# Kernel tuning notes

Measured on AMD Instinct MI355X. Metric: run time of the kernel, lower is better.

Reference implementation:

```python
import jax, jax.numpy as jnp
import numpy as np

H_IN = 1024
H_OUT = 1024
P = 512
DT_MIN = 0.004
DT_MAX = 0.1
STEP_RESCALE = 1.0
MIN_NEG = 1e-3
EPS_LAM = 1e-6
EPS_DIV = 1e-9
CLIP_MAX = 20.0


def _hippo_lambda_raw(p):
    # Mirrors TorchS5.__init__ HiPPO-LegS-style symmetric init.
    idx = np.arange(p, dtype=np.float64)
    Pv = np.sqrt(1.0 + 2.0 * idx)
    A = np.tril(Pv[:, None] * Pv[None, :]) - np.diag(idx)
    A = -A
    Pr = np.sqrt(idx + 0.5)
    S = A + Pr[:, None] * Pr[None, :]
    S_sym = 0.5 * (S + S.T)
    eig = np.linalg.eigvalsh(S_sym).astype(np.float32)
    lambda_init = -np.clip(np.abs(eig), 1e-3, None)
    raw = -np.log(np.expm1(np.clip(-lambda_init, 1e-6, None)))
    return jnp.asarray(raw, dtype=jnp.float32)


def setup_inputs() -> dict:
    key = jax.random.key(0)
    ku, kt, kb, kc = jax.random.split(key, 4)
    Bsz, L = 16, 1024
    u = jax.random.normal(ku, (Bsz, L, H_IN), dtype=jnp.float32)
    timesteps = jax.random.uniform(kt, (Bsz, L), dtype=jnp.float32)
    Lambda_raw = _hippo_lambda_raw(P)
    log_step_init = 0.5 * (np.log(DT_MIN) + np.log(DT_MAX))
    log_step = jnp.full((P,), log_step_init, dtype=jnp.float32)
    # kaiming_uniform_(a=sqrt(5)) -> U(-1/sqrt(fan_in), 1/sqrt(fan_in))
    Bmat = jax.random.uniform(kb, (P, H_IN), dtype=jnp.float32,
                              minval=-1.0, maxval=1.0) / np.sqrt(H_IN)
    Cmat = jax.random.uniform(kc, (H_OUT, P), dtype=jnp.float32,
                              minval=-1.0, maxval=1.0) / np.sqrt(P)
    Dvec = jnp.zeros((H_IN,), dtype=jnp.float32)  # H_in == H_out path
    return {"u": u, "timesteps": timesteps, "Lambda_raw": Lambda_raw,
            "log_step": log_step, "B": Bmat, "C": Cmat, "D": Dvec}


def reference(u, timesteps, Lambda_raw, log_step, B, C, D):
    # u: [B,L,H_in], timesteps: [B,L]
    Bu = jnp.einsum('ph,blh->blp', B, u)                      # [B,L,P]
    step_vec = STEP_RESCALE * jnp.exp(log_step)               # [P]
    Lam = -(jax.nn.softplus(Lambda_raw) + MIN_NEG)            # [P]
    Delta = jnp.maximum(step_vec[None, None, :] * timesteps[..., None], 0.0)
    A_bar = jnp.exp(jnp.minimum(Lam[None, None, :] * Delta, CLIP_MAX))
    # zoh gamma: (exp(Lam*Delta)-1)/Lam, fallback Delta near Lam=0
    gamma = jnp.where(jnp.abs(Lam)[None, None, :] > EPS_LAM,
                      (A_bar - 1.0) / Lam[None, None, :], Delta)
    b_seq = gamma * Bu
    A_cum = jnp.cumprod(A_bar, axis=1)                        # [B,L,P]
    z = b_seq / (A_cum + EPS_DIV)
    s = jnp.cumsum(z, axis=1)
    x_seq = A_cum * s
    ys = jnp.einsum('hp,blp->blh', C, x_seq) + D * u          # [B,L,H_out]
    return ys
```

## Files before the change

### kernel.cpp

```cpp
#include <hip/hip_runtime.h>
#include <cstdint>
#include <cstddef>

#define H_IN   1024
#define H_OUTD 1024
#define PDIM   512
#define BSZ    16
#define LSEQ   1024
#define BLM    (BSZ * LSEQ)
#define CCH    32
#define CLEN   32

typedef __bf16 bf16_t;
typedef __bf16 bf16x8 __attribute__((ext_vector_type(8)));
typedef float  floatx4 __attribute__((ext_vector_type(4)));

__device__ __forceinline__ unsigned short f2bf(float f) {
    unsigned u = __float_as_uint(f);
    u = u + 0x7fffu + ((u >> 16) & 1u);
    return (unsigned short)(u >> 16);
}
__device__ __forceinline__ float bf2f(unsigned short s) {
    return __uint_as_float((unsigned)s << 16);
}

__device__ __forceinline__ void gl_lds16(const void* g, void* l) {
    __builtin_amdgcn_global_load_lds(
        (const __attribute__((address_space(1))) void*)g,
        (__attribute__((address_space(3))) void*)l, 16, 0, 0);
}

#define NU4 (BLM * H_IN / 4)
#define NB4 (PDIM * H_IN / 4)
#define NC4 (H_OUTD * PDIM / 4)
__global__ void setup_kernel(const float* __restrict__ Lraw,
                             const float* __restrict__ lstep,
                             float* __restrict__ stepv,
                             float* __restrict__ lamv,
                             const float4* __restrict__ Usrc,
                             ushort4* __restrict__ Udst,
                             const float4* __restrict__ Bsrc,
                             ushort4* __restrict__ Bdst,
                             const float4* __restrict__ Csrc,
                             ushort4* __restrict__ Cdst) {
    const int gid = blockIdx.x * 256 + threadIdx.x;
    if (gid < PDIM) {
        stepv[gid] = expf(lstep[gid]);
        float x = Lraw[gid];
        float sp = fmaxf(x, 0.0f) + log1pf(expf(-fabsf(x)));
        lamv[gid] = -(sp + 1e-3f);
    }
    if (gid < NU4) {
        float4 v = Usrc[gid];
        ushort4 o;
        o.x = f2bf(v.x); o.y = f2bf(v.y); o.z = f2bf(v.z); o.w = f2bf(v.w);
        Udst[gid] = o;
    } else {
        const int g2 = gid - NU4;
        if (g2 < NB4) {
            float4 v = Bsrc[g2];
            ushort4 o;
            o.x = f2bf(v.x); o.y = f2bf(v.y); o.z = f2bf(v.z); o.w = f2bf(v.w);
            Bdst[g2] = o;
        } else if (g2 < NB4 + NC4) {
            const int g3 = g2 - NB4;
            float4 v = Csrc[g3];
            ushort4 o;
            o.x = f2bf(v.x); o.y = f2bf(v.y); o.z = f2bf(v.z); o.w = f2bf(v.w);
            Cdst[g3] = o;
        }
    }
}

template<int EPI, int OUTBF, int GXL>
__global__ __launch_bounds__(256, 4)
void gemm_nt(const bf16_t* __restrict__ A, const bf16_t* __restrict__ Bm,
             float* __restrict__ Cf, unsigned short* __restrict__ Cb,
             int M, int N, int K,
             const float* __restrict__ Dv, const unsigned short* __restrict__ U) {
    __shared__ bf16_t As[2 * 128 * 32];
    __shared__ bf16_t Bs[2 * 128 * 32];

    const int i     = blockIdx.x;
    const int n_blk = (i >> 3) & ((1 << GXL) - 1);
    const int m_blk = ((i >> (3 + GXL)) << 3) | (i & 7);
    const int m0    = m_blk << 7;
    const int n0    = n_blk << 7;

    const int tid  = threadIdx.x;
    const int lane = tid & 63;
    const int w    = tid >> 6;
    const int wm   = (w & 1) << 6;
    const int wn   = (w >> 1) << 6;
    const int r16  = lane & 15;
    const int q    = lane >> 4;
    const int fsw  = (q ^ (r16 & 3)) << 3;

    const int srow = lane >> 2;
    const int seg  = (lane & 3) ^ (srow & 3);
    const int c0   = w * 32;
    const int c1   = c0 + 16;

    const bf16_t* gA0 = A  + (size_t)(m0 + c0 + srow) * K + seg * 8;
    const bf16_t* gA1 = A  + (size_t)(m0 + c1 + srow) * K + seg * 8;
    const bf16_t* gB0 = Bm + (size_t)(n0 + c0 + srow) * K + seg * 8;
    const bf16_t* gB1 = Bm + (size_t)(n0 + c1 + srow) * K + seg * 8;
    bf16_t* lA0 = &As[c0 * 32];
    bf16_t* lA1 = &As[c1 * 32];
    bf16_t* lB0 = &Bs[c0 * 32];
    bf16_t* lB1 = &Bs[c1 * 32];

    floatx4 acc[4][4] = {};

    gl_lds16(gA0, lA0);
    gl_lds16(gA1, lA1);
    gl_lds16(gB0, lB0);
    gl_lds16(gB1, lB1);
    __syncthreads();

    int cur = 0;
    for (int k0 = 0; k0 < K; k0 += 32) {
        const int nxt = cur ^ 1;
        if (k0 + 32 < K) {
            gl_lds16(gA0 + k0 + 32, lA0 + nxt * 4096);
            gl_lds16(gA1 + k0 + 32, lA1 + nxt * 4096);
            gl_lds16(gB0 + k0 + 32, lB0 + nxt * 4096);
            gl_lds16(gB1 + k0 + 32, lB1 + nxt * 4096);
        }

        const bf16_t* rA = As + cur * 4096;
        const bf16_t* rB = Bs + cur * 4096;
        bf16x8 af[4], bfr[4];
#pragma unroll
        for (int ii = 0; ii < 4; ++ii) {
            af[ii]  = *(const bf16x8*)&rA[(wm + ii * 16 + r16) * 32 + fsw];
            bfr[ii] = *(const bf16x8*)&rB[(wn + ii * 16 + r16) * 32 + fsw];
        }
#pragma unroll
        for (int mi = 0; mi < 4; ++mi)
#pragma unroll
            for (int ni = 0; ni < 4; ++ni)
                acc[mi][ni] = __builtin_amdgcn_mfma_f32_16x16x32_bf16(
                    af[mi], bfr[ni], acc[mi][ni], 0, 0, 0);

        __syncthreads();
        cur = nxt;
    }

    float dn[4];
    if (EPI == 1) {
#pragma unroll
        for (int ni = 0; ni < 4; ++ni) dn[ni] = Dv[n0 + wn + ni * 16 + r16];
    }
#pragma unroll
    for (int mi = 0; mi < 4; ++mi) {
#pragma unroll
        for (int e = 0; e < 4; ++e) {
            const int m = m0 + wm + mi * 16 + q * 4 + e;
#pragma unroll
            for (int ni = 0; ni < 4; ++ni) {
                const int n = n0 + wn + ni * 16 + r16;
                const size_t idx = (size_t)m * N + n;
                float v = acc[mi][ni][e];
                if (EPI == 1) v += dn[ni] * bf2f(U[idx]);
                if (OUTBF == 1) Cb[idx] = f2bf(v);
                else            Cf[idx] = v;
            }
        }
    }
}

__global__ __launch_bounds__(512)
void scan_part1(const unsigned short* __restrict__ Bu, const float* __restrict__ ts,
                const float* __restrict__ stepv, const float* __restrict__ lamv,
                float* __restrict__ Pagg, float* __restrict__ Sagg) {
    const int c = blockIdx.x;
    const int b = blockIdx.y;
    const int p = threadIdx.x;

    const float lam  = lamv[p];
    const float stp  = stepv[p];
    const float rlam = 1.0f / lam;
    const bool  lam_big = fabsf(lam) > 1e-6f;

    const unsigned short* bu = Bu + ((size_t)b * LSEQ + c * CLEN) * PDIM + p;
    const float* tb = ts + b * LSEQ + c * CLEN;

    float P = 1.0f, S = 0.0f;
#pragma unroll 8
    for (int i = 0; i < CLEN; ++i) {
        float t     = tb[i];
        float delta = fmaxf(stp * t, 0.0f);
        float e     = fminf(lam * delta, 20.0f);
        float abar  = __expf(e);
        float gamma = lam_big ? (abar - 1.0f) * rlam : delta;
        S = fmaf(abar, S, gamma * bf2f(bu[(size_t)i * PDIM]));
        P *= abar;
    }
    const size_t o = ((size_t)b * CCH + c) * PDIM + p;
    Pagg[o] = P;
    Sagg[o] = S;
}

__global__ __launch_bounds__(512)
void scan_part23(const unsigned short* __restrict__ Bu, const float* __restrict__ ts,
                 const float* __restrict__ stepv, const float* __restrict__ lamv,
                 const float* __restrict__ Pagg, const float* __restrict__ Sagg,
                 unsigned short* __restrict__ Xbf) {
    const int c = blockIdx.x;
    const int b = blockIdx.y;
    const int p = threadIdx.x;

    const float lam  = lamv[p];
    const float stp  = stepv[p];
    const float rlam = 1.0f / lam;
    const bool  lam_big = fabsf(lam) > 1e-6f;

    const float* Pb = Pagg + (size_t)b * CCH * PDIM + p;
    const float* Sb = Sagg + (size_t)b * CCH * PDIM + p;
    float x = 0.0f;
    int cc = 0;
    for (; cc + 4 <= c; cc += 4) {
        float p0 = Pb[(size_t)(cc + 0) * PDIM], s0 = Sb[(size_t)(cc + 0) * PDIM];
        float p1 = Pb[(size_t)(cc + 1) * PDIM], s1 = Sb[(size_t)(cc + 1) * PDIM];
        float p2 = Pb[(size_t)(cc + 2) * PDIM], s2 = Sb[(size_t)(cc + 2) * PDIM];
        float p3 = Pb[(size_t)(cc + 3) * PDIM], s3 = Sb[(size_t)(cc + 3) * PDIM];
        float p01 = p0 * p1, s01 = fmaf(s0, p1, s1);
        float p23 = p2 * p3, s23 = fmaf(s2, p3, s3);
        float pq  = p01 * p23, sq = fmaf(s01, p23, s23);
        x = fmaf(pq, x, sq);
    }
    for (; cc < c; ++cc) {
        x = fmaf(Pb[(size_t)cc * PDIM], x, Sb[(size_t)cc * PDIM]);
    }

    const unsigned short* bu = Bu + ((size_t)b * LSEQ + c * CLEN) * PDIM + p;
    const float* tb = ts + b * LSEQ + c * CLEN;
    unsigned short* xo = Xbf + ((size_t)b * LSEQ + c * CLEN) * PDIM + p;

#pragma unroll 8
    for (int i = 0; i < CLEN; ++i) {
        float t     = tb[i];
        float delta = fmaxf(stp * t, 0.0f);
        float e     = fminf(lam * delta, 20.0f);
        float abar  = __expf(e);
        float gamma = lam_big ? (abar - 1.0f) * rlam : delta;
        x = fmaf(abar, x, gamma * bf2f(bu[(size_t)i * PDIM]));
        xo[(size_t)i * PDIM] = f2bf(x);
    }
}

extern "C" void kernel_launch(void* const* d_in, const int* in_sizes, int n_in,
                              void* d_out, int out_size, void* d_ws, size_t ws_size,
                              hipStream_t stream) {
    (void)in_sizes; (void)n_in; (void)out_size; (void)ws_size;
    const float* u  = (const float*)d_in[0];
    const float* ts = (const float*)d_in[1];
    const float* Lr = (const float*)d_in[2];
    const float* ls = (const float*)d_in[3];
    const float* Bm = (const float*)d_in[4];
    const float* Cm = (const float*)d_in[5];
    const float* Dv = (const float*)d_in[6];
    float* out = (float*)d_out;

    char* ws = (char*)d_ws;
    bf16_t*         u_bf = (bf16_t*)(ws);
    bf16_t*         B_bf = (bf16_t*)(ws + (32u << 20));
    bf16_t*         C_bf = (bf16_t*)(ws + (33u << 20));
    unsigned short* Bu   = (unsigned short*)(ws + (34u << 20));
    unsigned short* X_bf = (unsigned short*)(ws + (50u << 20));
    float*          Pagg = (float*)(ws + (66u << 20));
    float*          Sagg = (float*)(ws + (67u << 20));
    float*          stepv= (float*)(ws + (69u << 20));
    float*          lamv = stepv + PDIM;

    setup_kernel<<<(NU4 + NB4 + NC4) / 256, 256, 0, stream>>>(
        Lr, ls, stepv, lamv,
        (const float4*)u,  (ushort4*)u_bf,
        (const float4*)Bm, (ushort4*)B_bf,
        (const float4*)Cm, (ushort4*)C_bf);

    gemm_nt<0, 1, 2><<<512, 256, 0, stream>>>(
        u_bf, B_bf, nullptr, Bu, BLM, PDIM, H_IN, nullptr, nullptr);

    scan_part1<<<dim3(CCH, BSZ), 512, 0, stream>>>(Bu, ts, stepv, lamv, Pagg, Sagg);
    scan_part23<<<dim3(CCH, BSZ), 512, 0, stream>>>(Bu, ts, stepv, lamv,
                                                    Pagg, Sagg, X_bf);

    gemm_nt<1, 0, 3><<<1024, 256, 0, stream>>>(
        (const bf16_t*)X_bf, C_bf, out, nullptr, BLM, H_OUTD, PDIM, Dv,
        (const unsigned short*)u_bf);
}
```

Baseline: 192.8 us.

## Triple-buffer GEMM LDS tiles with prefetch depth two and skip zero-D epilogue loads

```diff
diff --git a/kernel.cpp b/kernel.cpp
--- a/kernel.cpp
+++ b/kernel.cpp
@@ -73,13 +73,13 @@
 }
 
 template<int EPI, int OUTBF, int GXL>
-__global__ __launch_bounds__(256, 4)
+__global__ __launch_bounds__(256, 3)
 void gemm_nt(const bf16_t* __restrict__ A, const bf16_t* __restrict__ Bm,
              float* __restrict__ Cf, unsigned short* __restrict__ Cb,
              int M, int N, int K,
              const float* __restrict__ Dv, const unsigned short* __restrict__ U) {
-    __shared__ bf16_t As[2 * 128 * 32];
-    __shared__ bf16_t Bs[2 * 128 * 32];
+    __shared__ bf16_t As[3 * 4096];
+    __shared__ bf16_t Bs[3 * 4096];
 
     const int i     = blockIdx.x;
     const int n_blk = (i >> 3) & ((1 << GXL) - 1);
@@ -112,24 +112,38 @@
 
     floatx4 acc[4][4] = {};
 
+    const int nk = K >> 5;
+
     gl_lds16(gA0, lA0);
     gl_lds16(gA1, lA1);
     gl_lds16(gB0, lB0);
     gl_lds16(gB1, lB1);
-    __syncthreads();
-
-    int cur = 0;
-    for (int k0 = 0; k0 < K; k0 += 32) {
-        const int nxt = cur ^ 1;
-        if (k0 + 32 < K) {
-            gl_lds16(gA0 + k0 + 32, lA0 + nxt * 4096);
-            gl_lds16(gA1 + k0 + 32, lA1 + nxt * 4096);
-            gl_lds16(gB0 + k0 + 32, lB0 + nxt * 4096);
-            gl_lds16(gB1 + k0 + 32, lB1 + nxt * 4096);
+    {
+        const int off = 32;
+        gl_lds16(gA0 + off, lA0 + 4096);
+        gl_lds16(gA1 + off, lA1 + 4096);
+        gl_lds16(gB0 + off, lB0 + 4096);
+        gl_lds16(gB1 + off, lB1 + 4096);
+    }
+
+    int rd = 0;
+    int wr = 2;
+    for (int kk = 0; kk < nk; ++kk) {
+        if (kk + 1 < nk) asm volatile("s_waitcnt vmcnt(4)" ::: "memory");
+        else             asm volatile("s_waitcnt vmcnt(0)" ::: "memory");
+        __builtin_amdgcn_s_barrier();
+
+        if (kk + 2 < nk) {
+            const int off = (kk + 2) << 5;
+            gl_lds16(gA0 + off, lA0 + wr * 4096);
+            gl_lds16(gA1 + off, lA1 + wr * 4096);
+            gl_lds16(gB0 + off, lB0 + wr * 4096);
+            gl_lds16(gB1 + off, lB1 + wr * 4096);
+            wr = (wr + 1 == 3) ? 0 : wr + 1;
         }
 
-        const bf16_t* rA = As + cur * 4096;
-        const bf16_t* rB = Bs + cur * 4096;
+        const bf16_t* rA = As + rd * 4096;
+        const bf16_t* rB = Bs + rd * 4096;
         bf16x8 af[4], bfr[4];
 #pragma unroll
         for (int ii = 0; ii < 4; ++ii) {
@@ -143,8 +157,7 @@
                 acc[mi][ni] = __builtin_amdgcn_mfma_f32_16x16x32_bf16(
                     af[mi], bfr[ni], acc[mi][ni], 0, 0, 0);
 
-        __syncthreads();
-        cur = nxt;
+        rd = (rd + 1 == 3) ? 0 : rd + 1;
     }
 
     float dn[4];
@@ -162,7 +175,9 @@
                 const int n = n0 + wn + ni * 16 + r16;
                 const size_t idx = (size_t)m * N + n;
                 float v = acc[mi][ni][e];
-                if (EPI == 1) v += dn[ni] * bf2f(U[idx]);
+                if (EPI == 1) {
+                    if (dn[ni] != 0.0f) v += dn[ni] * bf2f(U[idx]);
+                }
                 if (OUTBF == 1) Cb[idx] = f2bf(v);
                 else            Cf[idx] = v;
             }
```

After: 194.6 us. Within noise of the previous version (+0.9%).

## Fuse fp32-to-bf16 conversion of u into the first GEMM's A-tile load

Applied to the files above, without the earlier changes.

```diff
diff --git a/kernel.cpp b/kernel.cpp
--- a/kernel.cpp
+++ b/kernel.cpp
@@ -23,6 +23,9 @@
 __device__ __forceinline__ float bf2f(unsigned short s) {
     return __uint_as_float((unsigned)s << 16);
 }
+__device__ __forceinline__ unsigned pk2(float lo, float hi) {
+    return (unsigned)f2bf(lo) | ((unsigned)f2bf(hi) << 16);
+}
 
 __device__ __forceinline__ void gl_lds16(const void* g, void* l) {
     __builtin_amdgcn_global_load_lds(
@@ -30,15 +33,12 @@
         (__attribute__((address_space(3))) void*)l, 16, 0, 0);
 }
 
-#define NU4 (BLM * H_IN / 4)
 #define NB4 (PDIM * H_IN / 4)
 #define NC4 (H_OUTD * PDIM / 4)
 __global__ void setup_kernel(const float* __restrict__ Lraw,
                              const float* __restrict__ lstep,
                              float* __restrict__ stepv,
                              float* __restrict__ lamv,
-                             const float4* __restrict__ Usrc,
-                             ushort4* __restrict__ Udst,
                              const float4* __restrict__ Bsrc,
                              ushort4* __restrict__ Bdst,
                              const float4* __restrict__ Csrc,
@@ -50,20 +50,14 @@
         float sp = fmaxf(x, 0.0f) + log1pf(expf(-fabsf(x)));
         lamv[gid] = -(sp + 1e-3f);
     }
-    if (gid < NU4) {
-        float4 v = Usrc[gid];
+    if (gid < NB4) {
+        float4 v = Bsrc[gid];
         ushort4 o;
         o.x = f2bf(v.x); o.y = f2bf(v.y); o.z = f2bf(v.z); o.w = f2bf(v.w);
-        Udst[gid] = o;
+        Bdst[gid] = o;
     } else {
-        const int g2 = gid - NU4;
-        if (g2 < NB4) {
-            float4 v = Bsrc[g2];
-            ushort4 o;
-            o.x = f2bf(v.x); o.y = f2bf(v.y); o.z = f2bf(v.z); o.w = f2bf(v.w);
-            Bdst[g2] = o;
-        } else if (g2 < NB4 + NC4) {
-            const int g3 = g2 - NB4;
+        const int g3 = gid - NB4;
+        if (g3 < NC4) {
             float4 v = Csrc[g3];
             ushort4 o;
             o.x = f2bf(v.x); o.y = f2bf(v.y); o.z = f2bf(v.z); o.w = f2bf(v.w);
@@ -72,14 +66,12 @@
     }
 }
 
-template<int EPI, int OUTBF, int GXL>
-__global__ __launch_bounds__(256, 4)
-void gemm_nt(const bf16_t* __restrict__ A, const bf16_t* __restrict__ Bm,
-             float* __restrict__ Cf, unsigned short* __restrict__ Cb,
-             int M, int N, int K,
-             const float* __restrict__ Dv, const unsigned short* __restrict__ U) {
-    __shared__ bf16_t As[2 * 128 * 32];
-    __shared__ bf16_t Bs[2 * 128 * 32];
+template<int GXL>
+__global__ __launch_bounds__(256, 3)
+void gemm1_a32(const float* __restrict__ A32, const bf16_t* __restrict__ Bm,
+               unsigned short* __restrict__ Cb, int M, int N, int K) {
+    __shared__ bf16_t As[2 * 4096];
+    __shared__ bf16_t Bs[2 * 4096];
 
     const int i     = blockIdx.x;
     const int n_blk = (i >> 3) & ((1 << GXL) - 1);
@@ -100,6 +92,117 @@
     const int seg  = (lane & 3) ^ (srow & 3);
     const int c0   = w * 32;
     const int c1   = c0 + 16;
+    const bf16_t* gB0 = Bm + (size_t)(n0 + c0 + srow) * K + seg * 8;
+    const bf16_t* gB1 = Bm + (size_t)(n0 + c1 + srow) * K + seg * 8;
+    bf16_t* lB0 = &Bs[c0 * 32];
+    bf16_t* lB1 = &Bs[c1 * 32];
+
+    const int srow2 = lane >> 1;
+    const int halfk = lane & 1;
+    const int arow  = c0 + srow2;
+    const float* gA = A32 + (size_t)(m0 + arow) * K + halfk * 16;
+    const int sl0 = ((2 * halfk)     ^ (srow2 & 3)) * 8;
+    const int sl1 = ((2 * halfk + 1) ^ (srow2 & 3)) * 8;
+
+    floatx4 acc[4][4] = {};
+    float4 av[4];
+
+#pragma unroll
+    for (int j = 0; j < 4; ++j) av[j] = *(const float4*)(gA + j * 4);
+    gl_lds16(gB0, lB0);
+    gl_lds16(gB1, lB1);
+    {
+        uint4 u0, u1;
+        u0.x = pk2(av[0].x, av[0].y); u0.y = pk2(av[0].z, av[0].w);
+        u0.z = pk2(av[1].x, av[1].y); u0.w = pk2(av[1].z, av[1].w);
+        u1.x = pk2(av[2].x, av[2].y); u1.y = pk2(av[2].z, av[2].w);
+        u1.z = pk2(av[3].x, av[3].y); u1.w = pk2(av[3].z, av[3].w);
+        *(uint4*)&As[arow * 32 + sl0] = u0;
+        *(uint4*)&As[arow * 32 + sl1] = u1;
+    }
+    __syncthreads();
+
+    int cur = 0;
+    for (int k0 = 0; k0 < K; k0 += 32) {
+        const int nxt = cur ^ 1;
+        const bool pf = (k0 + 32 < K);
+        if (pf) {
+#pragma unroll
+            for (int j = 0; j < 4; ++j)
+                av[j] = *(const float4*)(gA + k0 + 32 + j * 4);
+            gl_lds16(gB0 + k0 + 32, lB0 + nxt * 4096);
+            gl_lds16(gB1 + k0 + 32, lB1 + nxt * 4096);
+        }
+
+        const bf16_t* rA = As + cur * 4096;
+        const bf16_t* rB = Bs + cur * 4096;
+        bf16x8 af[4], bfr[4];
+#pragma unroll
+        for (int ii = 0; ii < 4; ++ii) {
+            af[ii]  = *(const bf16x8*)&rA[(wm + ii * 16 + r16) * 32 + fsw];
+            bfr[ii] = *(const bf16x8*)&rB[(wn + ii * 16 + r16) * 32 + fsw];
+        }
+#pragma unroll
+        for (int mi = 0; mi < 4; ++mi)
+#pragma unroll
+            for (int ni = 0; ni < 4; ++ni)
+                acc[mi][ni] = __builtin_amdgcn_mfma_f32_16x16x32_bf16(
+                    af[mi], bfr[ni], acc[mi][ni], 0, 0, 0);
+
+        if (pf) {
+            uint4 u0, u1;
+            u0.x = pk2(av[0].x, av[0].y); u0.y = pk2(av[0].z, av[0].w);
+            u0.z = pk2(av[1].x, av[1].y); u0.w = pk2(av[1].z, av[1].w);
+            u1.x = pk2(av[2].x, av[2].y); u1.y = pk2(av[2].z, av[2].w);
+            u1.z = pk2(av[3].x, av[3].y); u1.w = pk2(av[3].z, av[3].w);
+            *(uint4*)&As[nxt * 4096 + arow * 32 + sl0] = u0;
+            *(uint4*)&As[nxt * 4096 + arow * 32 + sl1] = u1;
+        }
+        __syncthreads();
+        cur = nxt;
+    }
+
+#pragma unroll
+    for (int mi = 0; mi < 4; ++mi) {
+#pragma unroll
+        for (int e = 0; e < 4; ++e) {
+            const int m = m0 + wm + mi * 16 + q * 4 + e;
+#pragma unroll
+            for (int ni = 0; ni < 4; ++ni) {
+                const int n = n0 + wn + ni * 16 + r16;
+                Cb[(size_t)m * N + n] = f2bf(acc[mi][ni][e]);
+            }
+        }
+    }
+}
+
+template<int GXL>
+__global__ __launch_bounds__(256, 4)
+void gemm2_nt(const bf16_t* __restrict__ A, const bf16_t* __restrict__ Bm,
+              float* __restrict__ Cf, int M, int N, int K,
+              const float* __restrict__ Dv, const float* __restrict__ U32) {
+    __shared__ bf16_t As[2 * 4096];
+    __shared__ bf16_t Bs[2 * 4096];
+
+    const int i     = blockIdx.x;
+    const int n_blk = (i >> 3) & ((1 << GXL) - 1);
+    const int m_blk = ((i >> (3 + GXL)) << 3) | (i & 7);
+    const int m0    = m_blk << 7;
+    const int n0    = n_blk << 7;
+
+    const int tid  = threadIdx.x;
+    const int lane = tid & 63;
+    const int w    = tid >> 6;
+    const int wm   = (w & 1) << 6;
+    const int wn   = (w >> 1) << 6;
+    const int r16  = lane & 15;
+    const int q    = lane >> 4;
+    const int fsw  = (q ^ (r16 & 3)) << 3;
+
+    const int srow = lane >> 2;
+    const int seg  = (lane & 3) ^ (srow & 3);
+    const int c0   = w * 32;
+    const int c1   = c0 + 16;
 
     const bf16_t* gA0 = A  + (size_t)(m0 + c0 + srow) * K + seg * 8;
     const bf16_t* gA1 = A  + (size_t)(m0 + c1 + srow) * K + seg * 8;
@@ -148,10 +251,8 @@
     }
 
     float dn[4];
-    if (EPI == 1) {
-#pragma unroll
-        for (int ni = 0; ni < 4; ++ni) dn[ni] = Dv[n0 + wn + ni * 16 + r16];
-    }
+#pragma unroll
+    for (int ni = 0; ni < 4; ++ni) dn[ni] = Dv[n0 + wn + ni * 16 + r16];
 #pragma unroll
     for (int mi = 0; mi < 4; ++mi) {
 #pragma unroll
@@ -162,9 +263,8 @@
                 const int n = n0 + wn + ni * 16 + r16;
                 const size_t idx = (size_t)m * N + n;
                 float v = acc[mi][ni][e];
-                if (EPI == 1) v += dn[ni] * bf2f(U[idx]);
-                if (OUTBF == 1) Cb[idx] = f2bf(v);
-                else            Cf[idx] = v;
+                if (dn[ni] != 0.0f) v += dn[ni] * U32[idx];
+                __builtin_nontemporal_store(v, &Cf[idx]);
             }
         }
     }
@@ -264,30 +364,27 @@
     float* out = (float*)d_out;
 
     char* ws = (char*)d_ws;
-    bf16_t*         u_bf = (bf16_t*)(ws);
-    bf16_t*         B_bf = (bf16_t*)(ws + (32u << 20));
-    bf16_t*         C_bf = (bf16_t*)(ws + (33u << 20));
-    unsigned short* Bu   = (unsigned short*)(ws + (34u << 20));
-    unsigned short* X_bf = (unsigned short*)(ws + (50u << 20));
-    float*          Pagg = (float*)(ws + (66u << 20));
-    float*          Sagg = (float*)(ws + (67u << 20));
-    float*          stepv= (float*)(ws + (69u << 20));
+    bf16_t*         B_bf = (bf16_t*)(ws);
+    bf16_t*         C_bf = (bf16_t*)(ws + (1u << 20));
+    unsigned short* Bu   = (unsigned short*)(ws + (2u << 20));
+    unsigned short* X_bf = (unsigned short*)(ws + (18u << 20));
+    float*          Pagg = (float*)(ws + (34u << 20));
+    float*          Sagg = (float*)(ws + (35u << 20));
+    float*          stepv= (float*)(ws + (36u << 20));
     float*          lamv = stepv + PDIM;
 
-    setup_kernel<<<(NU4 + NB4 + NC4) / 256, 256, 0, stream>>>(
+    setup_kernel<<<(NB4 + NC4) / 256, 256, 0, stream>>>(
         Lr, ls, stepv, lamv,
-        (const float4*)u,  (ushort4*)u_bf,
         (const float4*)Bm, (ushort4*)B_bf,
         (const float4*)Cm, (ushort4*)C_bf);
 
-    gemm_nt<0, 1, 2><<<512, 256, 0, stream>>>(
-        u_bf, B_bf, nullptr, Bu, BLM, PDIM, H_IN, nullptr, nullptr);
+    gemm1_a32<2><<<512, 256, 0, stream>>>(
+        u, B_bf, Bu, BLM, PDIM, H_IN);
 
     scan_part1<<<dim3(CCH, BSZ), 512, 0, stream>>>(Bu, ts, stepv, lamv, Pagg, Sagg);
     scan_part23<<<dim3(CCH, BSZ), 512, 0, stream>>>(Bu, ts, stepv, lamv,
                                                     Pagg, Sagg, X_bf);
 
-    gemm_nt<1, 0, 3><<<1024, 256, 0, stream>>>(
-        (const bf16_t*)X_bf, C_bf, out, nullptr, BLM, H_OUTD, PDIM, Dv,
-        (const unsigned short*)u_bf);
-}
+    gemm2_nt<3><<<1024, 256, 0, stream>>>(
+        (const bf16_t*)X_bf, C_bf, out, BLM, H_OUTD, PDIM, Dv, u);
+}
```

Measured after the change: 212.5 us. 1.1x slower.

## Shrink GEMM1 M tile to 64 and skip zero-D residual reads in GEMM2

Applied to the files above, without the earlier changes.

```diff
diff --git a/kernel.cpp b/kernel.cpp
--- a/kernel.cpp
+++ b/kernel.cpp
@@ -72,14 +72,99 @@
     }
 }
 
-template<int EPI, int OUTBF, int GXL>
+template<int GXL>
 __global__ __launch_bounds__(256, 4)
-void gemm_nt(const bf16_t* __restrict__ A, const bf16_t* __restrict__ Bm,
-             float* __restrict__ Cf, unsigned short* __restrict__ Cb,
-             int M, int N, int K,
-             const float* __restrict__ Dv, const unsigned short* __restrict__ U) {
-    __shared__ bf16_t As[2 * 128 * 32];
-    __shared__ bf16_t Bs[2 * 128 * 32];
+void gemm1_bm64(const bf16_t* __restrict__ A, const bf16_t* __restrict__ Bm,
+                unsigned short* __restrict__ Cb, int M, int N, int K) {
+    constexpr int ABUF = 64 * 32;
+    constexpr int BBUF = 128 * 32;
+    __shared__ bf16_t As[2 * ABUF];
+    __shared__ bf16_t Bs[2 * BBUF];
+
+    const int i     = blockIdx.x;
+    const int n_blk = (i >> 3) & ((1 << GXL) - 1);
+    const int m_blk = ((i >> (3 + GXL)) << 3) | (i & 7);
+    const int m0    = m_blk * 64;
+    const int n0    = n_blk << 7;
+
+    const int tid  = threadIdx.x;
+    const int lane = tid & 63;
+    const int w    = tid >> 6;
+    const int wm   = (w & 1) * 32;
+    const int wn   = (w >> 1) * 64;
+    const int r16  = lane & 15;
+    const int q    = lane >> 4;
+    const int fsw  = (q ^ (r16 & 3)) << 3;
+
+    const int srow = lane >> 2;
+    const int seg  = (lane & 3) ^ (srow & 3);
+    const int aro  = w * 16;
+    const int bc0  = w * 32;
+
+    const bf16_t* gA  = A  + (size_t)(m0 + aro + srow) * K + seg * 8;
+    const bf16_t* gB0 = Bm + (size_t)(n0 + bc0 + srow) * K + seg * 8;
+    const bf16_t* gB1 = Bm + (size_t)(n0 + bc0 + 16 + srow) * K + seg * 8;
+    bf16_t* lA  = &As[aro * 32];
+    bf16_t* lB0 = &Bs[bc0 * 32];
+    bf16_t* lB1 = &Bs[(bc0 + 16) * 32];
+
+    floatx4 acc[2][4] = {};
+
+    gl_lds16(gA,  lA);
+    gl_lds16(gB0, lB0);
+    gl_lds16(gB1, lB1);
+    __syncthreads();
+
+    int cur = 0;
+    for (int k0 = 0; k0 < K; k0 += 32) {
+        const int nxt = cur ^ 1;
+        if (k0 + 32 < K) {
+            gl_lds16(gA  + k0 + 32, lA  + nxt * ABUF);
+            gl_lds16(gB0 + k0 + 32, lB0 + nxt * BBUF);
+            gl_lds16(gB1 + k0 + 32, lB1 + nxt * BBUF);
+        }
+
+        const bf16_t* rA = As + cur * ABUF;
+        const bf16_t* rB = Bs + cur * BBUF;
+        bf16x8 af[2], bfr[4];
+#pragma unroll
+        for (int ii = 0; ii < 2; ++ii)
+            af[ii]  = *(const bf16x8*)&rA[(wm + ii * 16 + r16) * 32 + fsw];
+#pragma unroll
+        for (int ii = 0; ii < 4; ++ii)
+            bfr[ii] = *(const bf16x8*)&rB[(wn + ii * 16 + r16) * 32 + fsw];
+#pragma unroll
+        for (int mi = 0; mi < 2; ++mi)
+#pragma unroll
+            for (int ni = 0; ni < 4; ++ni)
+                acc[mi][ni] = __builtin_amdgcn_mfma_f32_16x16x32_bf16(
+                    af[mi], bfr[ni], acc[mi][ni], 0, 0, 0);
+
+        __syncthreads();
+        cur = nxt;
+    }
+
+#pragma unroll
+    for (int mi = 0; mi < 2; ++mi) {
+#pragma unroll
+        for (int e = 0; e < 4; ++e) {
+            const int m = m0 + wm + mi * 16 + q * 4 + e;
+#pragma unroll
+            for (int ni = 0; ni < 4; ++ni) {
+                const int n = n0 + wn + ni * 16 + r16;
+                Cb[(size_t)m * N + n] = f2bf(acc[mi][ni][e]);
+            }
+        }
+    }
+}
+
+template<int GXL>
+__global__ __launch_bounds__(256, 4)
+void gemm2_nt(const bf16_t* __restrict__ A, const bf16_t* __restrict__ Bm,
+              float* __restrict__ Cf, int M, int N, int K,
+              const float* __restrict__ Dv, const float* __restrict__ U32) {
+    __shared__ bf16_t As[2 * 4096];
+    __shared__ bf16_t Bs[2 * 4096];
 
     const int i     = blockIdx.x;
     const int n_blk = (i >> 3) & ((1 << GXL) - 1);
@@ -148,10 +233,8 @@
     }
 
     float dn[4];
-    if (EPI == 1) {
-#pragma unroll
-        for (int ni = 0; ni < 4; ++ni) dn[ni] = Dv[n0 + wn + ni * 16 + r16];
-    }
+#pragma unroll
+    for (int ni = 0; ni < 4; ++ni) dn[ni] = Dv[n0 + wn + ni * 16 + r16];
 #pragma unroll
     for (int mi = 0; mi < 4; ++mi) {
 #pragma unroll
@@ -162,9 +245,8 @@
                 const int n = n0 + wn + ni * 16 + r16;
                 const size_t idx = (size_t)m * N + n;
                 float v = acc[mi][ni][e];
-                if (EPI == 1) v += dn[ni] * bf2f(U[idx]);
-                if (OUTBF == 1) Cb[idx] = f2bf(v);
-                else            Cf[idx] = v;
+                if (dn[ni] != 0.0f) v += dn[ni] * U32[idx];
+                __builtin_nontemporal_store(v, &Cf[idx]);
             }
         }
     }
@@ -280,14 +362,13 @@
         (const float4*)Bm, (ushort4*)B_bf,
         (const float4*)Cm, (ushort4*)C_bf);
 
-    gemm_nt<0, 1, 2><<<512, 256, 0, stream>>>(
-        u_bf, B_bf, nullptr, Bu, BLM, PDIM, H_IN, nullptr, nullptr);
+    gemm1_bm64<2><<<1024, 256, 0, stream>>>(
+        u_bf, B_bf, Bu, BLM, PDIM, H_IN);
 
     scan_part1<<<dim3(CCH, BSZ), 512, 0, stream>>>(Bu, ts, stepv, lamv, Pagg, Sagg);
     scan_part23<<<dim3(CCH, BSZ), 512, 0, stream>>>(Bu, ts, stepv, lamv,
                                                     Pagg, Sagg, X_bf);
 
-    gemm_nt<1, 0, 3><<<1024, 256, 0, stream>>>(
-        (const bf16_t*)X_bf, C_bf, out, nullptr, BLM, H_OUTD, PDIM, Dv,
-        (const unsigned short*)u_bf);
-}
+    gemm2_nt<3><<<1024, 256, 0, stream>>>(
+        (const bf16_t*)X_bf, C_bf, out, BLM, H_OUTD, PDIM, Dv, u);
+}
```

New measurement: 195.6 us. Within noise of the previous version (+1.4%).
